# Kernel optimization log

Measured on AMD Instinct MI355X. Metric: run time of the kernel, lower is better.

Reference implementation:

```python
import jax, jax.numpy as jnp
import numpy as np

FLOW_NUM = 16


def _mlp(z0, p):
    # z0: [B,1]; p = (W1,b1,W2,b2,W3,b3,W4,b4)
    W1, b1, W2, b2, W3, b3, W4, b4 = p
    h = jax.nn.relu(z0 @ W1 + b1)      # [B,10]
    h = jax.nn.relu(h @ W2 + b2)       # [B,10]
    h = jnp.tanh(h @ W3 + b3)          # [B,20]
    return h @ W4 + b4                 # [B,2]


def _forward(inputs, W1, b1, W2, b2, W3, b3, W4, b4):
    x = inputs.astype(jnp.float32)
    z0 = x[:, 0:1]
    z1 = x[:, 1:2]

    def step(carry, p):
        z0_old, z1_old, logdet = carry
        out = _mlp(z0_old, p)                    # [B,2]
        log_scale = out[:, 0:1]                  # log of affine scale
        shift = out[:, 1:2]
        z1_new = jnp.exp(log_scale) * z1_old + shift
        # swap roles for next flow (as in the torch code)
        return (z1_new, z0_old, logdet + log_scale), None

    (z0f, z1f, logdet), _ = jax.lax.scan(
        step, (z0, z1, jnp.zeros_like(z0)), (W1, b1, W2, b2, W3, b3, W4, b4))
    # after the loop: z0_new = z0_old (carry[1]), z1_new = carry[0]
    z0_new, z1_new = z1f, z0f
    # log of standard-normal density product (same math as log(pz))
    log_pz = -0.5 * (z0_new ** 2 + z1_new ** 2) - jnp.log(2.0 * jnp.pi)
    return log_pz + logdet, jnp.concatenate((z0_new, z1_new), axis=1)


def setup_inputs() -> dict:
    key = jax.random.key(0)
    ks = jax.random.split(key, 9)
    B, F = 2097152, FLOW_NUM

    def glorot(k, shape):
        fan_in, fan_out = shape[-2], shape[-1]
        lim = np.sqrt(6.0 / (fan_in + fan_out))
        return jax.random.uniform(k, shape, jnp.float32, -lim, lim)

    return {
        "inputs": jax.random.normal(ks[0], (B, 2), jnp.float32),
        "W1": glorot(ks[1], (F, 1, 10)),  "b1": jnp.zeros((F, 10), jnp.float32),
        "W2": glorot(ks[2], (F, 10, 10)), "b2": jnp.zeros((F, 10), jnp.float32),
        "W3": glorot(ks[3], (F, 10, 20)), "b3": jnp.zeros((F, 20), jnp.float32),
        "W4": glorot(ks[4], (F, 20, 2)),  "b4": jnp.zeros((F, 2), jnp.float32),
    }


def reference(inputs, W1, b1, W2, b2, W3, b3, W4, b4):
    return _forward(inputs, W1, b1, W2, b2, W3, b3, W4, b4)
```

## Files before the change

kernel.cpp:

```cpp
#include <hip/hip_runtime.h>
#include <hip/hip_fp16.h>

#define FLOWS 16
#define NE 1024
#define TAB_QWORDS (FLOWS * NE)
#define TAB_BYTES  (TAB_QWORDS * 8)

#define TROWS 8
#define BLOCK 1024

__device__ __forceinline__ float tanh_fast(float x) {
    float e = __expf(2.0f * x);
    return 1.0f - 2.0f * __builtin_amdgcn_rcpf(e + 1.0f);
}

__device__ __forceinline__ float2 eval_mlp(int l, float z0,
        const float* __restrict__ W1, const float* __restrict__ B1,
        const float* __restrict__ W2, const float* __restrict__ B2,
        const float* __restrict__ W3, const float* __restrict__ B3,
        const float* __restrict__ W4, const float* __restrict__ B4) {
    const float* w1 = W1 + l * 10;
    const float* c1 = B1 + l * 10;
    const float* w2 = W2 + l * 100;
    const float* c2 = B2 + l * 10;
    const float* w3 = W3 + l * 200;
    const float* c3 = B3 + l * 20;
    const float* w4 = W4 + l * 40;
    const float* c4 = B4 + l * 2;

    float h1[10];
#pragma unroll
    for (int j = 0; j < 10; ++j)
        h1[j] = fmaxf(fmaf(z0, w1[j], c1[j]), 0.0f);

    float h2[10];
#pragma unroll
    for (int j = 0; j < 10; ++j) {
        float acc = c2[j];
#pragma unroll
        for (int i = 0; i < 10; ++i) acc = fmaf(h1[i], w2[i * 10 + j], acc);
        h2[j] = fmaxf(acc, 0.0f);
    }

    float h3[20];
#pragma unroll
    for (int j = 0; j < 20; ++j) {
        float acc = c3[j];
#pragma unroll
        for (int i = 0; i < 10; ++i) acc = fmaf(h2[i], w3[i * 20 + j], acc);
        h3[j] = tanh_fast(acc);
    }

    float ls = c4[0], sh = c4[1];
#pragma unroll
    for (int i = 0; i < 20; ++i) {
        ls = fmaf(h3[i], w4[i * 2 + 0], ls);
        sh = fmaf(h3[i], w4[i * 2 + 1], sh);
    }
    return make_float2(ls * 1.4426950408889634f, sh);
}

__device__ __forceinline__ float node_z0(int i) {
    float u = fmaf((float)i, 30.0f / 1024.0f, -15.0f);
    float m = 0.125f * (exp2f(fabsf(u)) - 1.0f);
    return u < 0.0f ? -m : m;
}

__device__ __forceinline__ unsigned int pack_h2(float a, float b) {
    unsigned int lo = (unsigned int)__half_as_ushort(__float2half_rn(a));
    unsigned int hi = (unsigned int)__half_as_ushort(__float2half_rn(b));
    return lo | (hi << 16);
}

__global__ __launch_bounds__(256) void build_table_d(
        const float* __restrict__ W1, const float* __restrict__ B1,
        const float* __restrict__ W2, const float* __restrict__ B2,
        const float* __restrict__ W3, const float* __restrict__ B3,
        const float* __restrict__ W4, const float* __restrict__ B4,
        uint2* __restrict__ gtab) {
    int t = blockIdx.x * blockDim.x + threadIdx.x;
    if (t >= TAB_QWORDS) return;
    int l = t >> 10, i = t & (NE - 1);
    float2 r0 = eval_mlp(l, node_z0(i),     W1, B1, W2, B2, W3, B3, W4, B4);
    float2 r1 = eval_mlp(l, node_z0(i + 1), W1, B1, W2, B2, W3, B3, W4, B4);
    float ls0 = __half2float(__float2half_rn(r0.x));
    float sh0 = __half2float(__float2half_rn(r0.y));
    float ls1 = __half2float(__float2half_rn(r1.x));
    float sh1 = __half2float(__float2half_rn(r1.y));
    uint2 e;
    e.x = pack_h2(ls0, sh0);
    e.y = pack_h2(ls1 - ls0, sh1 - sh0);
    gtab[t] = e;
}

typedef __fp16 pkrtz_t __attribute__((ext_vector_type(2)));

__global__ __launch_bounds__(BLOCK) void realnvp_lds64(
        const float* __restrict__ x,
        const uint2* __restrict__ gtab,
        float* __restrict__ out, int nrows) {
    __shared__ uint2 st[TAB_QWORDS];

    {
        uint4* d = (uint4*)st;
        const uint4* s = (const uint4*)gtab;
        for (int k = threadIdx.x; k < TAB_QWORDS / 2; k += BLOCK) d[k] = s[k];
    }
    __syncthreads();

    const int rbase = blockIdx.x * (TROWS * BLOCK) + threadIdx.x;

    float z0[TROWS], z1[TROWS], ld2[TROWS];
#pragma unroll
    for (int r = 0; r < TROWS; ++r) {
        const int row = rbase + r * BLOCK;
        float2 xv = (row < nrows) ? reinterpret_cast<const float2*>(x)[row]
                                  : make_float2(0.0f, 0.0f);
        z0[r] = xv.x; z1[r] = xv.y; ld2[r] = 0.0f;
    }

    const float INV_DU = 1024.0f / 30.0f;

#pragma unroll 1
    for (int l = 0; l < FLOWS; ++l) {
        const uint2* tf = st + (l << 10);

        int idx[TROWS]; float fr[TROWS];
#pragma unroll
        for (int r = 0; r < TROWS; ++r) {
            float a  = fmaf(fabsf(z0[r]), 8.0f, 1.0f);
            float lg = __log2f(a);
            float u  = copysignf(lg, z0[r]);
            float fi = fmaf(u, INV_DU, 512.0f);
            fi = fminf(fmaxf(fi, 0.0f), 1023.99f);
            float t = truncf(fi);
            idx[r] = (int)t;
            fr[r]  = fi - t;
        }

        uint2 e[TROWS];
#pragma unroll
        for (int r = 0; r < TROWS; ++r)
            e[r] = tf[idx[r]];

#pragma unroll
        for (int r = 0; r < TROWS; ++r) {
            pkrtz_t fr2 = __builtin_amdgcn_cvt_pkrtz(fr[r], fr[r]);
            __half2 frh, base, del;
            __builtin_memcpy(&frh,  &fr2,    4);
            __builtin_memcpy(&base, &e[r].x, 4);
            __builtin_memcpy(&del,  &e[r].y, 4);
            __half2 v = __hfma2(frh, del, base);
            float ls2 = __half2float(__low2half(v));
            float sh  = __half2float(__high2half(v));
            float t   = fmaf(exp2f(ls2), z1[r], sh);
            z1[r] = z0[r];
            z0[r] = t;
            ld2[r] += ls2;
        }
    }

    float* out_lp = out;
    float2* out_z = reinterpret_cast<float2*>(out + nrows);
#pragma unroll
    for (int r = 0; r < TROWS; ++r) {
        const int row = rbase + r * BLOCK;
        if (row < nrows) {
            const float z0n = z1[r], z1n = z0[r];
            const float ld  = ld2[r] * 0.6931471805599453f;
            const float lp  = fmaf(-0.5f, fmaf(z0n, z0n, z1n * z1n), -1.8378770664093453f) + ld;
            out_lp[row] = lp;
            out_z[row]  = make_float2(z0n, z1n);
        }
    }
}

extern "C" void kernel_launch(void* const* d_in, const int* in_sizes, int n_in,
                              void* d_out, int out_size, void* d_ws, size_t ws_size,
                              hipStream_t stream) {
    const float* x  = (const float*)d_in[0];
    const float* W1 = (const float*)d_in[1];
    const float* B1 = (const float*)d_in[2];
    const float* W2 = (const float*)d_in[3];
    const float* B2 = (const float*)d_in[4];
    const float* W3 = (const float*)d_in[5];
    const float* B3 = (const float*)d_in[6];
    const float* W4 = (const float*)d_in[7];
    const float* B4 = (const float*)d_in[8];
    const int nrows = in_sizes[0] / 2;

    uint2* gtab = (uint2*)d_ws;
    build_table_d<<<(TAB_QWORDS + 255) / 256, 256, 0, stream>>>(
        W1, B1, W2, B2, W3, B3, W4, B4, gtab);

    const int rows_per_block = TROWS * BLOCK;
    const int blocks = (nrows + rows_per_block - 1) / rows_per_block;
    realnvp_lds64<<<blocks, BLOCK, 0, stream>>>(x, gtab, (float*)d_out, nrows);
}
```

Measured before the change: 37.82 us.

## Index lookup table via float bit patterns instead of log2 and truncation

The table grid changes from a log2-spaced uniform grid to one indexed directly by the exponent/mantissa bits of 1+8|z|. Each lookup's index and fraction then come from integer shifts and masks instead of a log2, clamp and trunc, and the sign handling becomes an XOR on a centered table pointer. The flow loop is also fully unrolled in pairs so the z0/z1 swaps disappear, and a min-blocks hint is added to the launch bounds. The grid resolution now follows the float mantissa bits, which shifts the interpolation accuracy profile, and full unrolling grows code size and register pressure.

```diff
diff --git a/kernel.cpp b/kernel.cpp
--- a/kernel.cpp
+++ b/kernel.cpp
@@ -6,8 +6,8 @@
 #define TAB_QWORDS (FLOWS * NE)
 #define TAB_BYTES  (TAB_QWORDS * 8)
 
+#define BLOCK 1024
 #define TROWS 8
-#define BLOCK 1024
 
 __device__ __forceinline__ float tanh_fast(float x) {
     float e = __expf(2.0f * x);
@@ -60,42 +60,45 @@
     return make_float2(ls * 1.4426950408889634f, sh);
 }
 
-__device__ __forceinline__ float node_z0(int i) {
-    float u = fmaf((float)i, 30.0f / 1024.0f, -15.0f);
-    float m = 0.125f * (exp2f(fabsf(u)) - 1.0f);
-    return u < 0.0f ? -m : m;
+__device__ __forceinline__ float node_from_t(unsigned t, bool neg) {
+    float a = __uint_as_float(0x3F800000u + t);
+    float m = 0.125f * (a - 1.0f);
+    return neg ? -m : m;
 }
 
 __device__ __forceinline__ unsigned int pack_h2(float a, float b) {
-    unsigned int lo = (unsigned int)__half_as_ushort(__float2half_rn(a));
-    unsigned int hi = (unsigned int)__half_as_ushort(__float2half_rn(b));
+    unsigned int lo = (unsigned int)(__half_as_ushort(__float2half_rn(a)));
+    unsigned int hi = (unsigned int)(__half_as_ushort(__float2half_rn(b)));
     return lo | (hi << 16);
 }
 
-__global__ __launch_bounds__(256) void build_table_d(
+__global__ __launch_bounds__(256) void build_table_bits(
         const float* __restrict__ W1, const float* __restrict__ B1,
         const float* __restrict__ W2, const float* __restrict__ B2,
         const float* __restrict__ W3, const float* __restrict__ B3,
         const float* __restrict__ W4, const float* __restrict__ B4,
         uint2* __restrict__ gtab) {
-    int t = blockIdx.x * blockDim.x + threadIdx.x;
-    if (t >= TAB_QWORDS) return;
-    int l = t >> 10, i = t & (NE - 1);
-    float2 r0 = eval_mlp(l, node_z0(i),     W1, B1, W2, B2, W3, B3, W4, B4);
-    float2 r1 = eval_mlp(l, node_z0(i + 1), W1, B1, W2, B2, W3, B3, W4, B4);
-    float ls0 = __half2float(__float2half_rn(r0.x));
-    float sh0 = __half2float(__float2half_rn(r0.y));
-    float ls1 = __half2float(__float2half_rn(r1.x));
-    float sh1 = __half2float(__float2half_rn(r1.y));
+    int tid = blockIdx.x * blockDim.x + threadIdx.x;
+    if (tid >= TAB_QWORDS) return;
+    int l = tid >> 10, idx = tid & (NE - 1);
+    bool neg = idx < 512;
+    unsigned ia = neg ? (unsigned)(511 - idx) : (unsigned)(idx - 512);
+    unsigned t0 = ia << 18, t1 = (ia + 1u) << 18;
+    float2 f0 = eval_mlp(l, node_from_t(t0, neg), W1, B1, W2, B2, W3, B3, W4, B4);
+    float2 f1 = eval_mlp(l, node_from_t(t1, neg), W1, B1, W2, B2, W3, B3, W4, B4);
+    float ls0 = __half2float(__float2half_rn(f0.x));
+    float sh0 = __half2float(__float2half_rn(f0.y));
+    float ls1 = __half2float(__float2half_rn(f1.x));
+    float sh1 = __half2float(__float2half_rn(f1.y));
     uint2 e;
     e.x = pack_h2(ls0, sh0);
     e.y = pack_h2(ls1 - ls0, sh1 - sh0);
-    gtab[t] = e;
+    gtab[tid] = e;
 }
 
 typedef __fp16 pkrtz_t __attribute__((ext_vector_type(2)));
 
-__global__ __launch_bounds__(BLOCK) void realnvp_lds64(
+__global__ __launch_bounds__(BLOCK, 4) void realnvp_bits(
         const float* __restrict__ x,
         const uint2* __restrict__ gtab,
         float* __restrict__ out, int nrows) {
@@ -104,45 +107,43 @@
     {
         uint4* d = (uint4*)st;
         const uint4* s = (const uint4*)gtab;
-        for (int k = threadIdx.x; k < TAB_QWORDS / 2; k += BLOCK) d[k] = s[k];
+#pragma unroll
+        for (int k = 0; k < TAB_QWORDS / 2; k += BLOCK)
+            d[k + threadIdx.x] = s[k + threadIdx.x];
     }
     __syncthreads();
 
     const int rbase = blockIdx.x * (TROWS * BLOCK) + threadIdx.x;
 
-    float z0[TROWS], z1[TROWS], ld2[TROWS];
+    float z0[TROWS], z1[TROWS], ldS[TROWS];
 #pragma unroll
     for (int r = 0; r < TROWS; ++r) {
         const int row = rbase + r * BLOCK;
         float2 xv = (row < nrows) ? reinterpret_cast<const float2*>(x)[row]
                                   : make_float2(0.0f, 0.0f);
-        z0[r] = xv.x; z1[r] = xv.y; ld2[r] = 0.0f;
-    }
-
-    const float INV_DU = 1024.0f / 30.0f;
-
-#pragma unroll 1
-    for (int l = 0; l < FLOWS; ++l) {
-        const uint2* tf = st + (l << 10);
-
-        int idx[TROWS]; float fr[TROWS];
+        z0[r] = xv.x; z1[r] = xv.y; ldS[r] = 0.0f;
+    }
+
+    auto step = [&](int l, const float* zi, const float* zm, float* zo) {
+        const uint2* tf = st + (l << 10) + 512;
+        int   io[TROWS];
+        float fr[TROWS];
 #pragma unroll
         for (int r = 0; r < TROWS; ++r) {
-            float a  = fmaf(fabsf(z0[r]), 8.0f, 1.0f);
-            float lg = __log2f(a);
-            float u  = copysignf(lg, z0[r]);
-            float fi = fmaf(u, INV_DU, 512.0f);
-            fi = fminf(fmaxf(fi, 0.0f), 1023.99f);
-            float t = truncf(fi);
-            idx[r] = (int)t;
-            fr[r]  = fi - t;
+            float z = zi[r];
+            float a = fmaf(fabsf(z), 8.0f, 1.0f);
+            unsigned b = __float_as_uint(a);
+            b = b < 0x477FFFFFu ? b : 0x477FFFFFu;
+            unsigned t = b - 0x3F800000u;
+            unsigned ia = t >> 18;
+            int m = ((int)__float_as_uint(z)) >> 31;
+            io[r] = (int)(ia ^ (unsigned)m);
+            fr[r] = (float)(t & 0x3FFFFu) * 3.814697265625e-06f;
         }
-
         uint2 e[TROWS];
 #pragma unroll
         for (int r = 0; r < TROWS; ++r)
-            e[r] = tf[idx[r]];
-
+            e[r] = tf[io[r]];
 #pragma unroll
         for (int r = 0; r < TROWS; ++r) {
             pkrtz_t fr2 = __builtin_amdgcn_cvt_pkrtz(fr[r], fr[r]);
@@ -153,21 +154,29 @@
             __half2 v = __hfma2(frh, del, base);
             float ls2 = __half2float(__low2half(v));
             float sh  = __half2float(__high2half(v));
-            float t   = fmaf(exp2f(ls2), z1[r], sh);
-            z1[r] = z0[r];
-            z0[r] = t;
-            ld2[r] += ls2;
+            zo[r] = fmaf(exp2f(ls2), zm[r], sh);
+            ldS[r] += ls2;
         }
+    };
+
+    float w[TROWS], v[TROWS];
+#pragma unroll
+    for (int lp = 0; lp < FLOWS; lp += 2) {
+        step(lp,     z0, z1, w);
+        step(lp + 1, w,  z0, v);
+#pragma unroll
+        for (int r = 0; r < TROWS; ++r) { z0[r] = v[r]; z1[r] = w[r]; }
     }
 
     float* out_lp = out;
     float2* out_z = reinterpret_cast<float2*>(out + nrows);
+    const float LN2 = 0.6931471805599453f;
 #pragma unroll
     for (int r = 0; r < TROWS; ++r) {
         const int row = rbase + r * BLOCK;
         if (row < nrows) {
             const float z0n = z1[r], z1n = z0[r];
-            const float ld  = ld2[r] * 0.6931471805599453f;
+            const float ld  = ldS[r] * LN2;
             const float lp  = fmaf(-0.5f, fmaf(z0n, z0n, z1n * z1n), -1.8378770664093453f) + ld;
             out_lp[row] = lp;
             out_z[row]  = make_float2(z0n, z1n);
@@ -190,10 +199,10 @@
     const int nrows = in_sizes[0] / 2;
 
     uint2* gtab = (uint2*)d_ws;
-    build_table_d<<<(TAB_QWORDS + 255) / 256, 256, 0, stream>>>(
+    build_table_bits<<<(TAB_QWORDS + 255) / 256, 256, 0, stream>>>(
         W1, B1, W2, B2, W3, B3, W4, B4, gtab);
 
     const int rows_per_block = TROWS * BLOCK;
     const int blocks = (nrows + rows_per_block - 1) / rows_per_block;
-    realnvp_lds64<<<blocks, BLOCK, 0, stream>>>(x, gtab, (float*)d_out, nrows);
-}
+    realnvp_bits<<<blocks, BLOCK, 0, stream>>>(x, gtab, (float*)d_out, nrows);
+}
```

After: 44.28 us. +17.1%, slower.
